# Optimization experiments

Measured on AMD Instinct MI355X. Metric: run time of the kernel, lower is better.

Reference implementation:

```python
import jax, jax.numpy as jnp
import numpy as np

E = 1024      # embed_dim
H = 8         # att_heads
ALPHA = 1.3   # CELU alpha
EPS = 1e-5    # GroupNorm eps (torch default)


def _celu(x):
    return jnp.where(x > 0, x, ALPHA * jnp.expm1(x / ALPHA))


def _proj(x2d, W, b, gamma, beta):
    # Linear -> CELU(1.3) -> GroupNorm(H groups) over flattened tokens [N, E]
    y = x2d @ W.T + b
    y = _celu(y)
    N, C = y.shape
    yg = y.reshape(N, H, C // H)
    mu = yg.mean(-1, keepdims=True)
    var = yg.var(-1, keepdims=True)
    yn = ((yg - mu) * jax.lax.rsqrt(var + EPS)).reshape(N, C)
    return yn * gamma + beta


def setup_inputs() -> dict:
    key = jax.random.key(0)
    ks = jax.random.split(key, 16)
    B, M = 32, 1024
    inp = {
        'query':  jax.random.normal(ks[0], (B, M, E), jnp.float32),
        'key':    jax.random.normal(ks[1], (B, M, E), jnp.float32),
        'mask':   jnp.ones((B, M), jnp.int32),
        'value1': jax.random.normal(ks[2], (B, E), jnp.float32),
        'value2': jax.random.normal(ks[3], (B, M, E), jnp.float32),
    }
    def lin(k):
        return jax.random.normal(k, (E, E), jnp.float32) * 0.02
    inp.update({
        'Wq': lin(ks[4]),  'bq': jnp.zeros((E,), jnp.float32),
        'gq': jnp.ones((E,), jnp.float32), 'betaq': jnp.zeros((E,), jnp.float32),
        'Wk': lin(ks[5]),  'bk': jnp.zeros((E,), jnp.float32),
        'gk': jnp.ones((E,), jnp.float32), 'betak': jnp.zeros((E,), jnp.float32),
        'Wv': lin(ks[6]),  'bv': jnp.zeros((E,), jnp.float32),
        'gv': jnp.ones((E,), jnp.float32), 'betav': jnp.zeros((E,), jnp.float32),
        'Wm': lin(ks[7]),  'bm': jnp.zeros((E,), jnp.float32),
    })
    return inp


def reference(query, key, mask, value1, value2,
              Wq, bq, gq, betaq,
              Wk, bk, gk, betak,
              Wv, bv, gv, betav,
              Wm, bm):
    B, M, C = query.shape
    D = C // H
    scaling = D ** -0.5
    # value1 is intentionally unused (matches the original module)
    q = _proj(query.reshape(-1, C),  Wq, bq, gq, betaq).reshape(B, M, H, D).transpose(0, 2, 1, 3)
    k = _proj(key.reshape(-1, C),    Wk, bk, gk, betak).reshape(B, M, H, D).transpose(0, 2, 1, 3)
    v = _proj(value2.reshape(-1, C), Wv, bv, gv, betav).reshape(B, M, H, D).transpose(0, 2, 1, 3)
    scores = jnp.einsum('bhqd,bhkd->bhqk', q, k) * scaling
    scores = jnp.where(mask[:, None, None, :] == 0, jnp.float32(-1e9), scores)
    att = jax.nn.softmax(scores, axis=-1)
    out = jnp.einsum('bhqk,bhkd->bhqd', att, v)
    out = out.transpose(0, 2, 1, 3).reshape(B, M, C)
    return out @ Wm.T + bm
```

## Files before the change

### kernel.cpp

```cpp
#include <hip/hip_runtime.h>
#include <math.h>

#define E_DIM 1024
#define HH 8
#define DH 128
#define BB 32
#define MM 1024
#define NTOK 32768
#define CHUNK 16384
#define CELU_A 1.3f
#define GN_EPS 1e-5f
#define SCALE_F 0.08838834764831845f

typedef unsigned short ushort_t;
typedef __attribute__((ext_vector_type(8))) short short8;
typedef __attribute__((ext_vector_type(4))) float f32x4;

#define MFMA16(a,b,c) __builtin_amdgcn_mfma_f32_16x16x32_bf16((a),(b),(c),0,0,0)

union U8 { short8 v; ushort_t u[8]; };

__device__ __forceinline__ ushort_t f2bf(float f) {
    unsigned u = __float_as_uint(f);
    u += 0x7fffu + ((u >> 16) & 1u);
    return (ushort_t)(u >> 16);
}
__device__ __forceinline__ float bf2f(ushort_t h) {
    return __uint_as_float(((unsigned)h) << 16);
}

__device__ __forceinline__ void gload16(const void* g, void* l) {
    __builtin_amdgcn_global_load_lds(
        (const __attribute__((address_space(1))) unsigned*)g,
        (__attribute__((address_space(3))) unsigned*)l, 16, 0, 0);
}

__global__ __launch_bounds__(256)
void split_kernel(const float* __restrict__ in, ushort_t* __restrict__ hi,
                  ushort_t* __restrict__ lo, int n8)
{
    int i = blockIdx.x * 256 + threadIdx.x;
    if (i >= n8) return;
    const float4* p = (const float4*)in;
    float4 a = p[2 * i], b = p[2 * i + 1];
    float f[8] = {a.x, a.y, a.z, a.w, b.x, b.y, b.z, b.w};
    U8 h, l;
#pragma unroll
    for (int j = 0; j < 8; ++j) {
        ushort_t hh = f2bf(f[j]);
        h.u[j] = hh;
        l.u[j] = f2bf(f[j] - bf2f(hh));
    }
    *(short8*)&hi[(size_t)i * 8] = h.v;
    *(short8*)&lo[(size_t)i * 8] = l.v;
}

struct alignas(16) TilesT {
    ushort_t ahi[128 * 32]; ushort_t alo[128 * 32];
    ushort_t bhi[128 * 32]; ushort_t blo[128 * 32];
};
struct alignas(16) EpiT {
    float ybuf[64 * 132]; float mu[64]; float rs[64];
};
union SmemU { TilesT t; EpiT e; };

template<int MODE>
__global__ __launch_bounds__(256, 3)
void proj_kernel(const ushort_t* __restrict__ Ahi, const ushort_t* __restrict__ Alo,
                 const ushort_t* __restrict__ Bhi, const ushort_t* __restrict__ Blo,
                 const float* __restrict__ bias, const float* __restrict__ gamma,
                 const float* __restrict__ beta, int row_off,
                 ushort_t* __restrict__ out0, ushort_t* __restrict__ out1,
                 float* __restrict__ outf)
{
    __shared__ SmemU sm;

    const int tid  = threadIdx.x;
    const int w    = tid >> 6, lane = tid & 63;
    const int quad = lane >> 4, l16 = lane & 15;
    const int wr   = (w >> 1) * 64, wc = (w & 1) * 64;
    const int lrow0 = blockIdx.x * 128;
    const int row0  = row_off + lrow0;
    const int col0  = blockIdx.y * 128;

    f32x4 Cf[4][4];
#pragma unroll
    for (int i = 0; i < 4; ++i)
#pragma unroll
        for (int j = 0; j < 4; ++j) Cf[i][j] = (f32x4){0.f, 0.f, 0.f, 0.f};

    const int s0 = tid, s1 = tid + 256;
    const int ra0 = tid >> 2, ra1 = ra0 + 64;
    const int ga  = (tid & 3) * 8;

    unsigned aoff0 = 0, aoff1 = 0;
    size_t a2b0 = 0, a2b1 = 0;
    if constexpr (MODE == 2) {
        int n0 = row0 + ra0, n1 = row0 + ra1;
        a2b0 = ((size_t)(n0 >> 10) * (HH * MM) + (n0 & 1023)) * 256;
        a2b1 = ((size_t)(n1 >> 10) * (HH * MM) + (n1 & 1023)) * 256;
    } else {
        aoff0 = (unsigned)((lrow0 + ra0) * E_DIM + ga);
        aoff1 = (unsigned)((lrow0 + ra1) * E_DIM + ga);
    }
    const unsigned boff0 = (unsigned)((col0 + ra0) * E_DIM + ga);
    const unsigned boff1 = (unsigned)((col0 + ra1) * E_DIM + ga);

    for (int k0 = 0; k0 < E_DIM; k0 += 32) {
        if constexpr (MODE == 2) {
            int e0 = k0 + ga;
            size_t ao = (size_t)(e0 >> 7) * (MM * 256) + (e0 & 127);
            gload16(Ahi + a2b0 + ao,       &sm.t.ahi[s0 * 8]);
            gload16(Ahi + a2b0 + ao + 128, &sm.t.alo[s0 * 8]);
            gload16(Ahi + a2b1 + ao,       &sm.t.ahi[s1 * 8]);
            gload16(Ahi + a2b1 + ao + 128, &sm.t.alo[s1 * 8]);
        } else {
            gload16(Ahi + aoff0 + k0, &sm.t.ahi[s0 * 8]);
            gload16(Alo + aoff0 + k0, &sm.t.alo[s0 * 8]);
            gload16(Ahi + aoff1 + k0, &sm.t.ahi[s1 * 8]);
            gload16(Alo + aoff1 + k0, &sm.t.alo[s1 * 8]);
        }
        gload16(Bhi + boff0 + k0, &sm.t.bhi[s0 * 8]);
        gload16(Blo + boff0 + k0, &sm.t.blo[s0 * 8]);
        gload16(Bhi + boff1 + k0, &sm.t.bhi[s1 * 8]);
        gload16(Blo + boff1 + k0, &sm.t.blo[s1 * 8]);
        __syncthreads();
        short8 a_hi[4], a_lo[4], b_hi[4], b_lo[4];
#pragma unroll
        for (int mt = 0; mt < 4; ++mt) {
            int r = wr + mt * 16 + l16;
            a_hi[mt] = *(const short8*)&sm.t.ahi[r * 32 + quad * 8];
            a_lo[mt] = *(const short8*)&sm.t.alo[r * 32 + quad * 8];
        }
#pragma unroll
        for (int nt = 0; nt < 4; ++nt) {
            int r = wc + nt * 16 + l16;
            b_hi[nt] = *(const short8*)&sm.t.bhi[r * 32 + quad * 8];
            b_lo[nt] = *(const short8*)&sm.t.blo[r * 32 + quad * 8];
        }
#pragma unroll
        for (int mt = 0; mt < 4; ++mt)
#pragma unroll
            for (int nt = 0; nt < 4; ++nt) {
                f32x4 c = Cf[mt][nt];
                c = MFMA16(a_hi[mt], b_hi[nt], c);
                c = MFMA16(a_hi[mt], b_lo[nt], c);
                c = MFMA16(a_lo[mt], b_hi[nt], c);
                Cf[mt][nt] = c;
            }
        __syncthreads();
    }

    if constexpr (MODE == 2) {
#pragma unroll
        for (int mt = 0; mt < 4; ++mt)
#pragma unroll
            for (int nt = 0; nt < 4; ++nt) {
                int c = col0 + wc + nt * 16 + l16;
                float bv = bias[c];
#pragma unroll
                for (int reg = 0; reg < 4; ++reg) {
                    int r = row0 + wr + mt * 16 + quad * 4 + reg;
                    outf[(size_t)r * E_DIM + c] = Cf[mt][nt][reg] + bv;
                }
            }
    } else {
        for (int h2 = 0; h2 < 2; ++h2) {
            __syncthreads();
            if ((w >> 1) == h2) {
#pragma unroll
                for (int mt = 0; mt < 4; ++mt)
#pragma unroll
                    for (int nt = 0; nt < 4; ++nt) {
                        int c = wc + nt * 16 + l16;
                        float bv = bias[col0 + c];
#pragma unroll
                        for (int reg = 0; reg < 4; ++reg) {
                            int r = mt * 16 + quad * 4 + reg;
                            float x = Cf[mt][nt][reg] + bv;
                            x = x > 0.f ? x : CELU_A * (__expf(x * (1.0f / CELU_A)) - 1.0f);
                            sm.e.ybuf[r * 132 + c] = x;
                        }
                    }
            }
            __syncthreads();
            {
                int r = tid >> 2, sg = (tid & 3) * 32;
                float s = 0.f, ss = 0.f;
                for (int i = 0; i < 32; i += 4) {
                    float4 v = *(float4*)&sm.e.ybuf[r * 132 + sg + i];
                    s  += v.x + v.y + v.z + v.w;
                    ss += v.x * v.x + v.y * v.y + v.z * v.z + v.w * v.w;
                }
                s  += __shfl_xor(s, 1);  ss += __shfl_xor(ss, 1);
                s  += __shfl_xor(s, 2);  ss += __shfl_xor(ss, 2);
                if ((tid & 3) == 0) {
                    float mu  = s * (1.f / 128.f);
                    float var = ss * (1.f / 128.f) - mu * mu;
                    sm.e.mu[r] = mu;
                    sm.e.rs[r] = rsqrtf(var + GN_EPS);
                }
            }
            __syncthreads();
            if constexpr (MODE == 0) {
                int r = tid >> 2, sg = (tid & 3) * 32;
                int n = row0 + h2 * 64 + r, b = n >> 10, m = n & 1023, h = blockIdx.y;
                float mu = sm.e.mu[r], rs = sm.e.rs[r];
                ushort_t* orow = out0 + ((size_t)((b * HH + h) * MM + m)) * 256;
                for (int i0 = 0; i0 < 32; i0 += 8) {
                    U8 ph, pl;
#pragma unroll
                    for (int j = 0; j < 8; ++j) {
                        int c = sg + i0 + j;
                        float y = (sm.e.ybuf[r * 132 + c] - mu) * rs * gamma[col0 + c] + beta[col0 + c];
                        ushort_t hh = f2bf(y);
                        ph.u[j] = hh; pl.u[j] = f2bf(y - bf2f(hh));
                    }
                    *(short8*)&orow[sg + i0]       = ph.v;
                    *(short8*)&orow[128 + sg + i0] = pl.v;
                }
            } else {
                int d = tid >> 1, off = (tid & 1) * 32;
                int b = row0 >> 10, m0 = (row0 & 1023) + h2 * 64, h = blockIdx.y;
                float g = gamma[col0 + d], be = beta[col0 + d];
                size_t vbase = ((size_t)(b * HH + h) * DH + d) * MM + m0 + off;
                for (int i0 = 0; i0 < 32; i0 += 8) {
                    U8 ph, pl;
#pragma unroll
                    for (int j = 0; j < 8; ++j) {
                        int rl = off + i0 + j;
                        float y = (sm.e.ybuf[rl * 132 + d] - sm.e.mu[rl]) * sm.e.rs[rl] * g + be;
                        ushort_t hh = f2bf(y);
                        ph.u[j] = hh; pl.u[j] = f2bf(y - bf2f(hh));
                    }
                    *(short8*)&out0[vbase + i0] = ph.v;
                    *(short8*)&out1[vbase + i0] = pl.v;
                }
            }
        }
    }
}

__global__ __launch_bounds__(256, 2)
void attn_kernel(const ushort_t* __restrict__ qsp, const ushort_t* __restrict__ ksp,
                 const ushort_t* __restrict__ vhi_g, const ushort_t* __restrict__ vlo_g,
                 const int* __restrict__ mask, ushort_t* __restrict__ obuf)
{
    __shared__ __align__(16) ushort_t Ks_hi[32 * 136], Ks_lo[32 * 136];
    __shared__ __align__(16) ushort_t Vt_hi[128 * 40], Vt_lo[128 * 40];
    __shared__ float Ss[64 * 33];
    __shared__ __align__(16) ushort_t Phi_s[64 * 40], Plo_s[64 * 40];
    __shared__ __align__(16) int mask_s[1024];
    __shared__ float alpha_s[64], mrow[64], lrow[64];

    const int tid  = threadIdx.x;
    const int w    = tid >> 6, lane = tid & 63;
    const int quad = lane >> 4, l16 = lane & 15;
    const int q0 = blockIdx.x * 64, bh = blockIdx.y, b = bh >> 3;

    ((int4*)mask_s)[tid] = ((const int4*)(mask + (size_t)b * MM))[tid];
    if (tid < 64) { mrow[tid] = -3.0e38f; lrow[tid] = 0.f; }

    short8 qa_hi[4], qa_lo[4];
    {
        const ushort_t* qrow = qsp + ((size_t)bh * MM + q0 + w * 16 + l16) * 256;
#pragma unroll
        for (int kc = 0; kc < 4; ++kc) {
            qa_hi[kc] = *(const short8*)(qrow + kc * 32 + quad * 8);
            qa_lo[kc] = *(const short8*)(qrow + 128 + kc * 32 + quad * 8);
        }
    }
    f32x4 Of[8];
#pragma unroll
    for (int i = 0; i < 8; ++i) Of[i] = (f32x4){0.f, 0.f, 0.f, 0.f};
    __syncthreads();

    for (int kt = 0; kt < 32; ++kt) {
        {
            int j = tid >> 3, seg = tid & 7;
            const ushort_t* kr = ksp + ((size_t)bh * MM + kt * 32 + j) * 256 + seg * 16;
            short8 h0 = *(const short8*)(kr);
            short8 h1 = *(const short8*)(kr + 8);
            short8 l0 = *(const short8*)(kr + 128);
            short8 l1 = *(const short8*)(kr + 136);
            *(short8*)&Ks_hi[j * 136 + seg * 16 + 0] = h0;
            *(short8*)&Ks_hi[j * 136 + seg * 16 + 8] = h1;
            *(short8*)&Ks_lo[j * 136 + seg * 16 + 0] = l0;
            *(short8*)&Ks_lo[j * 136 + seg * 16 + 8] = l1;
        }
        {
            int d = tid >> 1, hf = tid & 1;
            size_t vb = ((size_t)bh * DH + d) * MM + kt * 32 + hf * 16;
            short8 v0 = *(const short8*)(vhi_g + vb);
            short8 v1 = *(const short8*)(vhi_g + vb + 8);
            short8 u0 = *(const short8*)(vlo_g + vb);
            short8 u1 = *(const short8*)(vlo_g + vb + 8);
            *(short8*)&Vt_hi[d * 40 + hf * 16 + 0] = v0;
            *(short8*)&Vt_hi[d * 40 + hf * 16 + 8] = v1;
            *(short8*)&Vt_lo[d * 40 + hf * 16 + 0] = u0;
            *(short8*)&Vt_lo[d * 40 + hf * 16 + 8] = u1;
        }
        __syncthreads();
        f32x4 Sf[2];
        Sf[0] = (f32x4){0.f, 0.f, 0.f, 0.f};
        Sf[1] = (f32x4){0.f, 0.f, 0.f, 0.f};
#pragma unroll
        for (int kc = 0; kc < 4; ++kc) {
#pragma unroll
            for (int ct = 0; ct < 2; ++ct) {
                const short8 kbh = *(const short8*)&Ks_hi[(ct * 16 + l16) * 136 + kc * 32 + quad * 8];
                const short8 kbl = *(const short8*)&Ks_lo[(ct * 16 + l16) * 136 + kc * 32 + quad * 8];
                f32x4 c = Sf[ct];
                c = MFMA16(qa_hi[kc], kbh, c);
                c = MFMA16(qa_hi[kc], kbl, c);
                c = MFMA16(qa_lo[kc], kbh, c);
                Sf[ct] = c;
            }
        }
#pragma unroll
        for (int ct = 0; ct < 2; ++ct)
#pragma unroll
            for (int reg = 0; reg < 4; ++reg)
                Ss[(w * 16 + quad * 4 + reg) * 33 + ct * 16 + l16] = Sf[ct][reg];
        __syncthreads();
        {
            int r = tid >> 2, cb = (tid & 3) * 8;
            float sv[8];
            float pm = -3.0e38f;
#pragma unroll
            for (int c = 0; c < 8; ++c) {
                float s = Ss[r * 33 + cb + c] * SCALE_F;
                if (mask_s[kt * 32 + cb + c] == 0) s = -1e9f;
                sv[c] = s;
                pm = fmaxf(pm, s);
            }
            pm = fmaxf(pm, __shfl_xor(pm, 1));
            pm = fmaxf(pm, __shfl_xor(pm, 2));
            float mo = mrow[r];
            float mx = fmaxf(mo, pm);
            float al = __expf(mo - mx);
            float ps = 0.f;
            U8 ph, pl;
#pragma unroll
            for (int c = 0; c < 8; ++c) {
                float p = __expf(sv[c] - mx);
                ps += p;
                ushort_t hh = f2bf(p);
                ph.u[c] = hh;
                pl.u[c] = f2bf(p - bf2f(hh));
            }
            *(short8*)&Phi_s[r * 40 + cb] = ph.v;
            *(short8*)&Plo_s[r * 40 + cb] = pl.v;
            ps += __shfl_xor(ps, 1);
            ps += __shfl_xor(ps, 2);
            if ((tid & 3) == 0) {
                mrow[r] = mx;
                alpha_s[r] = al;
                lrow[r] = lrow[r] * al + ps;
            }
        }
        __syncthreads();
        {
            float ar[4];
#pragma unroll
            for (int reg = 0; reg < 4; ++reg) ar[reg] = alpha_s[w * 16 + quad * 4 + reg];
            const short8 pah = *(const short8*)&Phi_s[(w * 16 + l16) * 40 + quad * 8];
            const short8 pal = *(const short8*)&Plo_s[(w * 16 + l16) * 40 + quad * 8];
#pragma unroll
            for (int ct = 0; ct < 8; ++ct) {
                f32x4 c = Of[ct];
#pragma unroll
                for (int reg = 0; reg < 4; ++reg) c[reg] *= ar[reg];
                const short8 vbh = *(const short8*)&Vt_hi[(ct * 16 + l16) * 40 + quad * 8];
                const short8 vbl = *(const short8*)&Vt_lo[(ct * 16 + l16) * 40 + quad * 8];
                c = MFMA16(pah, vbh, c);
                c = MFMA16(pah, vbl, c);
                c = MFMA16(pal, vbh, c);
                Of[ct] = c;
            }
        }
        __syncthreads();
    }
    {
        float li[4];
#pragma unroll
        for (int reg = 0; reg < 4; ++reg) li[reg] = 1.f / lrow[w * 16 + quad * 4 + reg];
#pragma unroll
        for (int ct = 0; ct < 8; ++ct)
#pragma unroll
            for (int reg = 0; reg < 4; ++reg) {
                float v = Of[ct][reg] * li[reg];
                ushort_t hh = f2bf(v);
                ushort_t ll = f2bf(v - bf2f(hh));
                size_t rb = ((size_t)bh * MM + q0 + w * 16 + quad * 4 + reg) * 256 + ct * 16 + l16;
                obuf[rb]       = hh;
                obuf[rb + 128] = ll;
            }
    }
}

extern "C" void kernel_launch(void* const* d_in, const int* in_sizes, int n_in,
                              void* d_out, int out_size, void* d_ws, size_t ws_size,
                              hipStream_t stream)
{
    const float* query  = (const float*)d_in[0];
    const float* key    = (const float*)d_in[1];
    const int*   mask   = (const int*)d_in[2];
    const float* value2 = (const float*)d_in[4];
    const float* Wq = (const float*)d_in[5];
    const float* bq = (const float*)d_in[6];
    const float* gq = (const float*)d_in[7];
    const float* betaq = (const float*)d_in[8];
    const float* Wk = (const float*)d_in[9];
    const float* bk = (const float*)d_in[10];
    const float* gk = (const float*)d_in[11];
    const float* betak = (const float*)d_in[12];
    const float* Wv = (const float*)d_in[13];
    const float* bv = (const float*)d_in[14];
    const float* gv = (const float*)d_in[15];
    const float* betav = (const float*)d_in[16];
    const float* Wm = (const float*)d_in[17];
    const float* bm = (const float*)d_in[18];
    float* out = (float*)d_out;

    ushort_t* qsp = (ushort_t*)d_ws;
    ushort_t* ksp = qsp + (size_t)67108864;
    ushort_t* vhi = ksp + (size_t)67108864;
    ushort_t* vlo = vhi + (size_t)33554432;

    ushort_t* ob   = (ushort_t*)d_out;
    ushort_t* xhi  = ob;
    ushort_t* xlo  = ob + (size_t)CHUNK * E_DIM;
    ushort_t* wkhi = ob + (size_t)2 * CHUNK * E_DIM;
    ushort_t* wklo = wkhi + (size_t)E_DIM * E_DIM;
    ushort_t* wvhi = qsp;
    ushort_t* wvlo = wvhi + (size_t)E_DIM * E_DIM;
    ushort_t* wqhi = ksp;
    ushort_t* wqlo = wqhi + (size_t)E_DIM * E_DIM;
    ushort_t* wmhi = ksp;
    ushort_t* wmlo = wmhi + (size_t)E_DIM * E_DIM;

    const int WN8 = (E_DIM * E_DIM) / 8;
    const int XN8 = (CHUNK * E_DIM) / 8;

    split_kernel<<<WN8 / 256, 256, 0, stream>>>(Wv, wvhi, wvlo, WN8);
    split_kernel<<<WN8 / 256, 256, 0, stream>>>(Wq, wqhi, wqlo, WN8);
    split_kernel<<<WN8 / 256, 256, 0, stream>>>(Wk, wkhi, wklo, WN8);

    dim3 gproj(CHUNK / 128, E_DIM / 128);

    for (int c = 0; c < 2; ++c) {
        split_kernel<<<XN8 / 256, 256, 0, stream>>>(value2 + (size_t)c * CHUNK * E_DIM, xhi, xlo, XN8);
        proj_kernel<1><<<gproj, 256, 0, stream>>>(xhi, xlo, wvhi, wvlo, bv, gv, betav,
                                                  c * CHUNK, vhi, vlo, nullptr);
    }
    for (int c = 0; c < 2; ++c) {
        split_kernel<<<XN8 / 256, 256, 0, stream>>>(query + (size_t)c * CHUNK * E_DIM, xhi, xlo, XN8);
        proj_kernel<0><<<gproj, 256, 0, stream>>>(xhi, xlo, wqhi, wqlo, bq, gq, betaq,
                                                  c * CHUNK, qsp, nullptr, nullptr);
    }
    for (int c = 0; c < 2; ++c) {
        split_kernel<<<XN8 / 256, 256, 0, stream>>>(key + (size_t)c * CHUNK * E_DIM, xhi, xlo, XN8);
        proj_kernel<0><<<gproj, 256, 0, stream>>>(xhi, xlo, wkhi, wklo, bk, gk, betak,
                                                  c * CHUNK, ksp, nullptr, nullptr);
    }

    attn_kernel<<<dim3(MM / 64, BB * HH), 256, 0, stream>>>(qsp, ksp, vhi, vlo, mask, qsp);

    split_kernel<<<WN8 / 256, 256, 0, stream>>>(Wm, wmhi, wmlo, WN8);
    proj_kernel<2><<<dim3(NTOK / 128, E_DIM / 128), 256, 0, stream>>>(
        qsp, nullptr, wmhi, wmlo, bm, nullptr, nullptr, 0, nullptr, nullptr, out);
}
```

Before: 2.224 ms.

## Register-prefetch K/V tiles, do softmax in MFMA registers, pack mask to bits

The attention kernel now loads the next K/V tile into registers while the current tile is computed, which takes one global-load round trip off the critical path each iteration. The online softmax runs directly on the MFMA accumulator layout using cross-lane shuffles, so the shared score buffer, per-row shared state and one barrier per iteration go away. The mask is packed into 32-bit words by a small extra kernel, blocks are remapped so heads of the same batch share a schedule window, and occupancy is raised to 3 blocks per SM. The costs are higher register pressure under the tighter launch bound, one more tiny launch, and scattered 2-byte stores of P into shared memory.

```diff
diff --git a/kernel.cpp b/kernel.cpp
--- a/kernel.cpp
+++ b/kernel.cpp
@@ -53,6 +53,16 @@
     }
     *(short8*)&hi[(size_t)i * 8] = h.v;
     *(short8*)&lo[(size_t)i * 8] = l.v;
+}
+
+__global__ __launch_bounds__(32)
+void pack_mask(const int* __restrict__ mask, unsigned* __restrict__ mbits)
+{
+    int b = blockIdx.x, t = threadIdx.x;
+    const int* mp = mask + (size_t)b * MM + t * 32;
+    unsigned v = 0;
+    for (int j = 0; j < 32; ++j) v |= (mp[j] != 0 ? 1u : 0u) << j;
+    mbits[b * 32 + t] = v;
 }
 
 struct alignas(16) TilesT {
@@ -241,25 +251,23 @@
     }
 }
 
-__global__ __launch_bounds__(256, 2)
+__global__ __launch_bounds__(256, 3)
 void attn_kernel(const ushort_t* __restrict__ qsp, const ushort_t* __restrict__ ksp,
                  const ushort_t* __restrict__ vhi_g, const ushort_t* __restrict__ vlo_g,
-                 const int* __restrict__ mask, ushort_t* __restrict__ obuf)
+                 const unsigned* __restrict__ mbits, ushort_t* __restrict__ obuf)
 {
     __shared__ __align__(16) ushort_t Ks_hi[32 * 136], Ks_lo[32 * 136];
     __shared__ __align__(16) ushort_t Vt_hi[128 * 40], Vt_lo[128 * 40];
-    __shared__ float Ss[64 * 33];
     __shared__ __align__(16) ushort_t Phi_s[64 * 40], Plo_s[64 * 40];
-    __shared__ __align__(16) int mask_s[1024];
-    __shared__ float alpha_s[64], mrow[64], lrow[64];
 
     const int tid  = threadIdx.x;
     const int w    = tid >> 6, lane = tid & 63;
     const int quad = lane >> 4, l16 = lane & 15;
-    const int q0 = blockIdx.x * 64, bh = blockIdx.y, b = bh >> 3;
-
-    ((int4*)mask_s)[tid] = ((const int4*)(mask + (size_t)b * MM))[tid];
-    if (tid < 64) { mrow[tid] = -3.0e38f; lrow[tid] = 0.f; }
+    const int lin = blockIdx.y * 16 + blockIdx.x;
+    const int idx = lin >> 3;
+    const int bh  = ((idx >> 4) << 3) | (lin & 7);
+    const int q0  = (idx & 15) * 64;
+    const int b   = bh >> 3;
 
     short8 qa_hi[4], qa_lo[4];
     {
@@ -273,34 +281,51 @@
     f32x4 Of[8];
 #pragma unroll
     for (int i = 0; i < 8; ++i) Of[i] = (f32x4){0.f, 0.f, 0.f, 0.f};
-    __syncthreads();
+    float mreg[4] = {-3.0e38f, -3.0e38f, -3.0e38f, -3.0e38f};
+    float lreg[4] = {0.f, 0.f, 0.f, 0.f};
+
+    const int kj = tid >> 3, kseg = tid & 7;
+    const ushort_t* kbase  = ksp   + ((size_t)bh * MM + kj) * 256 + kseg * 16;
+    const int vd = tid >> 1, vhf = tid & 1;
+    const ushort_t* vhbase = vhi_g + ((size_t)bh * DH + vd) * MM + vhf * 16;
+    const ushort_t* vlbase = vlo_g + ((size_t)bh * DH + vd) * MM + vhf * 16;
+
+    short8 ck0 = *(const short8*)(kbase);
+    short8 ck1 = *(const short8*)(kbase + 8);
+    short8 ck2 = *(const short8*)(kbase + 128);
+    short8 ck3 = *(const short8*)(kbase + 136);
+    short8 cv0 = *(const short8*)(vhbase);
+    short8 cv1 = *(const short8*)(vhbase + 8);
+    short8 cv2 = *(const short8*)(vlbase);
+    short8 cv3 = *(const short8*)(vlbase + 8);
+    unsigned mw = mbits[b << 5];
 
     for (int kt = 0; kt < 32; ++kt) {
+        *(short8*)&Ks_hi[kj * 136 + kseg * 16 + 0] = ck0;
+        *(short8*)&Ks_hi[kj * 136 + kseg * 16 + 8] = ck1;
+        *(short8*)&Ks_lo[kj * 136 + kseg * 16 + 0] = ck2;
+        *(short8*)&Ks_lo[kj * 136 + kseg * 16 + 8] = ck3;
+        *(short8*)&Vt_hi[vd * 40 + vhf * 16 + 0] = cv0;
+        *(short8*)&Vt_hi[vd * 40 + vhf * 16 + 8] = cv1;
+        *(short8*)&Vt_lo[vd * 40 + vhf * 16 + 0] = cv2;
+        *(short8*)&Vt_lo[vd * 40 + vhf * 16 + 8] = cv3;
+        __syncthreads();
         {
-            int j = tid >> 3, seg = tid & 7;
-            const ushort_t* kr = ksp + ((size_t)bh * MM + kt * 32 + j) * 256 + seg * 16;
-            short8 h0 = *(const short8*)(kr);
-            short8 h1 = *(const short8*)(kr + 8);
-            short8 l0 = *(const short8*)(kr + 128);
-            short8 l1 = *(const short8*)(kr + 136);
-            *(short8*)&Ks_hi[j * 136 + seg * 16 + 0] = h0;
-            *(short8*)&Ks_hi[j * 136 + seg * 16 + 8] = h1;
-            *(short8*)&Ks_lo[j * 136 + seg * 16 + 0] = l0;
-            *(short8*)&Ks_lo[j * 136 + seg * 16 + 8] = l1;
-        }
-        {
-            int d = tid >> 1, hf = tid & 1;
-            size_t vb = ((size_t)bh * DH + d) * MM + kt * 32 + hf * 16;
-            short8 v0 = *(const short8*)(vhi_g + vb);
-            short8 v1 = *(const short8*)(vhi_g + vb + 8);
-            short8 u0 = *(const short8*)(vlo_g + vb);
-            short8 u1 = *(const short8*)(vlo_g + vb + 8);
-            *(short8*)&Vt_hi[d * 40 + hf * 16 + 0] = v0;
-            *(short8*)&Vt_hi[d * 40 + hf * 16 + 8] = v1;
-            *(short8*)&Vt_lo[d * 40 + hf * 16 + 0] = u0;
-            *(short8*)&Vt_lo[d * 40 + hf * 16 + 8] = u1;
-        }
-        __syncthreads();
+            int ktn = (kt + 1) & 31;
+            const ushort_t* kp  = kbase  + (size_t)ktn * 8192;
+            ck0 = *(const short8*)(kp);
+            ck1 = *(const short8*)(kp + 8);
+            ck2 = *(const short8*)(kp + 128);
+            ck3 = *(const short8*)(kp + 136);
+            const ushort_t* vhp = vhbase + ktn * 32;
+            const ushort_t* vlp = vlbase + ktn * 32;
+            cv0 = *(const short8*)(vhp);
+            cv1 = *(const short8*)(vhp + 8);
+            cv2 = *(const short8*)(vlp);
+            cv3 = *(const short8*)(vlp + 8);
+        }
+        unsigned mw_cur = mw;
+        mw = mbits[(b << 5) | ((kt + 1) & 31)];
         f32x4 Sf[2];
         Sf[0] = (f32x4){0.f, 0.f, 0.f, 0.f};
         Sf[1] = (f32x4){0.f, 0.f, 0.f, 0.f};
@@ -317,60 +342,47 @@
                 Sf[ct] = c;
             }
         }
-#pragma unroll
-        for (int ct = 0; ct < 2; ++ct)
-#pragma unroll
-            for (int reg = 0; reg < 4; ++reg)
-                Ss[(w * 16 + quad * 4 + reg) * 33 + ct * 16 + l16] = Sf[ct][reg];
+        float al4[4];
+#pragma unroll
+        for (int reg = 0; reg < 4; ++reg) {
+            float s0 = Sf[0][reg] * SCALE_F;
+            float s1 = Sf[1][reg] * SCALE_F;
+            if (!((mw_cur >> l16) & 1u))        s0 = -1e9f;
+            if (!((mw_cur >> (16 + l16)) & 1u)) s1 = -1e9f;
+            float pm = fmaxf(s0, s1);
+            pm = fmaxf(pm, __shfl_xor(pm, 1));
+            pm = fmaxf(pm, __shfl_xor(pm, 2));
+            pm = fmaxf(pm, __shfl_xor(pm, 4));
+            pm = fmaxf(pm, __shfl_xor(pm, 8));
+            float mo = mreg[reg];
+            float mx = fmaxf(mo, pm);
+            float al = __expf(mo - mx);
+            float p0 = __expf(s0 - mx);
+            float p1 = __expf(s1 - mx);
+            float ps = p0 + p1;
+            ps += __shfl_xor(ps, 1);
+            ps += __shfl_xor(ps, 2);
+            ps += __shfl_xor(ps, 4);
+            ps += __shfl_xor(ps, 8);
+            mreg[reg] = mx;
+            lreg[reg] = lreg[reg] * al + ps;
+            al4[reg] = al;
+            int rr = (w << 4) + (quad << 2) + reg;
+            ushort_t h0 = f2bf(p0), h1 = f2bf(p1);
+            Phi_s[rr * 40 + l16]      = h0;
+            Phi_s[rr * 40 + 16 + l16] = h1;
+            Plo_s[rr * 40 + l16]      = f2bf(p0 - bf2f(h0));
+            Plo_s[rr * 40 + 16 + l16] = f2bf(p1 - bf2f(h1));
+        }
         __syncthreads();
         {
-            int r = tid >> 2, cb = (tid & 3) * 8;
-            float sv[8];
-            float pm = -3.0e38f;
-#pragma unroll
-            for (int c = 0; c < 8; ++c) {
-                float s = Ss[r * 33 + cb + c] * SCALE_F;
-                if (mask_s[kt * 32 + cb + c] == 0) s = -1e9f;
-                sv[c] = s;
-                pm = fmaxf(pm, s);
-            }
-            pm = fmaxf(pm, __shfl_xor(pm, 1));
-            pm = fmaxf(pm, __shfl_xor(pm, 2));
-            float mo = mrow[r];
-            float mx = fmaxf(mo, pm);
-            float al = __expf(mo - mx);
-            float ps = 0.f;
-            U8 ph, pl;
-#pragma unroll
-            for (int c = 0; c < 8; ++c) {
-                float p = __expf(sv[c] - mx);
-                ps += p;
-                ushort_t hh = f2bf(p);
-                ph.u[c] = hh;
-                pl.u[c] = f2bf(p - bf2f(hh));
-            }
-            *(short8*)&Phi_s[r * 40 + cb] = ph.v;
-            *(short8*)&Plo_s[r * 40 + cb] = pl.v;
-            ps += __shfl_xor(ps, 1);
-            ps += __shfl_xor(ps, 2);
-            if ((tid & 3) == 0) {
-                mrow[r] = mx;
-                alpha_s[r] = al;
-                lrow[r] = lrow[r] * al + ps;
-            }
-        }
-        __syncthreads();
-        {
-            float ar[4];
-#pragma unroll
-            for (int reg = 0; reg < 4; ++reg) ar[reg] = alpha_s[w * 16 + quad * 4 + reg];
             const short8 pah = *(const short8*)&Phi_s[(w * 16 + l16) * 40 + quad * 8];
             const short8 pal = *(const short8*)&Plo_s[(w * 16 + l16) * 40 + quad * 8];
 #pragma unroll
             for (int ct = 0; ct < 8; ++ct) {
                 f32x4 c = Of[ct];
 #pragma unroll
-                for (int reg = 0; reg < 4; ++reg) c[reg] *= ar[reg];
+                for (int reg = 0; reg < 4; ++reg) c[reg] *= al4[reg];
                 const short8 vbh = *(const short8*)&Vt_hi[(ct * 16 + l16) * 40 + quad * 8];
                 const short8 vbl = *(const short8*)&Vt_lo[(ct * 16 + l16) * 40 + quad * 8];
                 c = MFMA16(pah, vbh, c);
@@ -384,7 +396,7 @@
     {
         float li[4];
 #pragma unroll
-        for (int reg = 0; reg < 4; ++reg) li[reg] = 1.f / lrow[w * 16 + quad * 4 + reg];
+        for (int reg = 0; reg < 4; ++reg) li[reg] = 1.f / lreg[reg];
 #pragma unroll
         for (int ct = 0; ct < 8; ++ct)
 #pragma unroll
@@ -428,21 +440,23 @@
     ushort_t* vhi = ksp + (size_t)67108864;
     ushort_t* vlo = vhi + (size_t)33554432;
 
-    ushort_t* ob   = (ushort_t*)d_out;
-    ushort_t* xhi  = ob;
-    ushort_t* xlo  = ob + (size_t)CHUNK * E_DIM;
-    ushort_t* wkhi = ob + (size_t)2 * CHUNK * E_DIM;
-    ushort_t* wklo = wkhi + (size_t)E_DIM * E_DIM;
-    ushort_t* wvhi = qsp;
-    ushort_t* wvlo = wvhi + (size_t)E_DIM * E_DIM;
-    ushort_t* wqhi = ksp;
-    ushort_t* wqlo = wqhi + (size_t)E_DIM * E_DIM;
-    ushort_t* wmhi = ksp;
-    ushort_t* wmlo = wmhi + (size_t)E_DIM * E_DIM;
+    ushort_t* ob    = (ushort_t*)d_out;
+    ushort_t* xhi   = ob;
+    ushort_t* xlo   = ob + (size_t)CHUNK * E_DIM;
+    ushort_t* wkhi  = ob + (size_t)2 * CHUNK * E_DIM;
+    ushort_t* wklo  = wkhi + (size_t)E_DIM * E_DIM;
+    unsigned* mbits = (unsigned*)(ob + (size_t)41943040);
+    ushort_t* wvhi  = qsp;
+    ushort_t* wvlo  = wvhi + (size_t)E_DIM * E_DIM;
+    ushort_t* wqhi  = ksp;
+    ushort_t* wqlo  = wqhi + (size_t)E_DIM * E_DIM;
+    ushort_t* wmhi  = ksp;
+    ushort_t* wmlo  = wmhi + (size_t)E_DIM * E_DIM;
 
     const int WN8 = (E_DIM * E_DIM) / 8;
     const int XN8 = (CHUNK * E_DIM) / 8;
 
+    pack_mask<<<BB, 32, 0, stream>>>(mask, mbits);
     split_kernel<<<WN8 / 256, 256, 0, stream>>>(Wv, wvhi, wvlo, WN8);
     split_kernel<<<WN8 / 256, 256, 0, stream>>>(Wq, wqhi, wqlo, WN8);
     split_kernel<<<WN8 / 256, 256, 0, stream>>>(Wk, wkhi, wklo, WN8);
@@ -465,7 +479,7 @@
                                                   c * CHUNK, ksp, nullptr, nullptr);
     }
 
-    attn_kernel<<<dim3(MM / 64, BB * HH), 256, 0, stream>>>(qsp, ksp, vhi, vlo, mask, qsp);
+    attn_kernel<<<dim3(MM / 64, BB * HH), 256, 0, stream>>>(qsp, ksp, vhi, vlo, mbits, qsp);
 
     split_kernel<<<WN8 / 256, 256, 0, stream>>>(Wm, wmhi, wmlo, WN8);
     proj_kernel<2><<<dim3(NTOK / 128, E_DIM / 128), 256, 0, stream>>>(
```

Result: no change. 2.190 ms (-1.5%).
